# Kernel optimization log

Measured on AMD Instinct MI355X. Metric: run time of the kernel, lower is better.

Reference implementation:

```python
import jax, jax.numpy as jnp
import numpy as np

B, T, DF, S = 64, 16, 512, 196      # batch, ticks, backbone channels, tokens
D_IN, H = 512, 8                     # attention embed dim, heads
DH = D_IN // H
DM, MEM, HN = 1024, 25, 32           # d_model neurons, memory length, NLM hidden
NSA, NSO, DOUT = 512, 512, 512       # sync sizes (random-pairing), output dim


def _ln(x, g, b, eps=1e-5):
    m = x.mean(-1, keepdims=True)
    v = ((x - m) ** 2).mean(-1, keepdims=True)
    return (x - m) / jnp.sqrt(v + eps) * g + b


def setup_inputs() -> dict:
    key = jax.random.key(0)
    ks = jax.random.split(key, 24)
    rn = lambda k, sh, sc: jax.random.normal(k, sh, jnp.float32) * sc
    p = {}
    p['x'] = rn(ks[0], (B, T, DF, S), 1.0)
    # q_proj (LazyLinear: n_sync_action -> d_input)
    p['Wqp'] = rn(ks[1], (NSA, D_IN), (1.0 / NSA) ** 0.5); p['bqp'] = jnp.zeros((D_IN,))
    # kv_proj: LazyLinear(DF->D_IN) + LayerNorm
    p['Wkv'] = rn(ks[2], (DF, D_IN), (1.0 / DF) ** 0.5); p['bkv'] = jnp.zeros((D_IN,))
    p['g_kv'] = jnp.ones((D_IN,)); p['b_kv'] = jnp.zeros((D_IN,))
    # MultiheadAttention projections
    sc = (1.0 / D_IN) ** 0.5
    p['Wq'] = rn(ks[3], (D_IN, D_IN), sc); p['bq'] = jnp.zeros((D_IN,))
    p['Wk'] = rn(ks[4], (D_IN, D_IN), sc); p['bk'] = jnp.zeros((D_IN,))
    p['Wv'] = rn(ks[5], (D_IN, D_IN), sc); p['bv'] = jnp.zeros((D_IN,))
    p['Wo'] = rn(ks[6], (D_IN, D_IN), sc); p['bo'] = jnp.zeros((D_IN,))
    # synapses: Linear(D_IN+DM -> 2*DM) + GLU + LayerNorm(DM)
    p['Wsyn'] = rn(ks[7], (D_IN + DM, 2 * DM), (1.0 / (D_IN + DM)) ** 0.5)
    p['bsyn'] = jnp.zeros((2 * DM,))
    p['g_syn'] = jnp.ones((DM,)); p['b_syn'] = jnp.zeros((DM,))
    # NLM: per-neuron 2-layer MLP over memory window
    p['W1'] = rn(ks[8], (DM, MEM, HN), (1.0 / MEM) ** 0.5); p['b1'] = jnp.zeros((DM, HN))
    p['W2'] = rn(ks[9], (DM, HN), (1.0 / HN) ** 0.5); p['b2'] = jnp.zeros((DM,))
    # learned initial states
    p['init_act'] = rn(ks[10], (DM,), (1.0 / DM) ** 0.5)
    p['init_hist'] = rn(ks[11], (DM, MEM), (1.0 / (DM + MEM)) ** 0.5)
    # decay params (init zero in torch)
    p['decay_a'] = jnp.zeros((NSA,)); p['decay_o'] = jnp.zeros((NSO,))
    # output projection (LazyLinear: n_sync_out -> d_output)
    p['Wout'] = rn(ks[12], (NSO, DOUT), (1.0 / NSO) ** 0.5); p['bout'] = jnp.zeros((DOUT,))
    # random-pairing neuron indices (buffers, constants)
    p['li_a'] = jax.random.randint(ks[13], (NSA,), 0, DM, jnp.int32)
    p['ri_a'] = jax.random.randint(ks[14], (NSA,), 0, DM, jnp.int32)
    p['li_o'] = jax.random.randint(ks[15], (NSO,), 0, DM, jnp.int32)
    p['ri_o'] = jax.random.randint(ks[16], (NSO,), 0, DM, jnp.int32)
    return p


def reference(x, Wqp, bqp, Wkv, bkv, g_kv, b_kv, Wq, bq, Wk, bk, Wv, bv, Wo, bo,
              Wsyn, bsyn, g_syn, b_syn, W1, b1, W2, b2, init_act, init_hist,
              decay_a, decay_o, Wout, bout, li_a, ri_a, li_o, ri_o):
    r_a = jnp.exp(-jnp.clip(decay_a, 0.0, 15.0))   # [NSA]
    r_o = jnp.exp(-jnp.clip(decay_o, 0.0, 15.0))   # [NSO]
    act0 = jnp.broadcast_to(init_act, (B, DM))
    hist0 = jnp.broadcast_to(init_hist, (B, DM, MEM))
    # initial 'out' sync state (decay_alpha=pairwise, decay_beta=ones)
    ao0 = act0[:, li_o] * act0[:, ri_o]
    bo0 = jnp.ones_like(ao0)
    # 'action' state starts None -> zeros so first update gives alpha=pairwise, beta=1
    aa0 = jnp.zeros((B, NSA), x.dtype); ba0 = jnp.zeros((B, NSA), x.dtype)

    def mha(q, kv):
        # q [B,1,D_IN], kv [B,S,D_IN]
        qh = (q @ Wq + bq).reshape(B, 1, H, DH)
        kh = (kv @ Wk + bk).reshape(B, S, H, DH)
        vh = (kv @ Wv + bv).reshape(B, S, H, DH)
        sc = jnp.einsum('bqhd,bkhd->bhqk', qh, kh) / jnp.sqrt(jnp.float32(DH))
        a = jax.nn.softmax(sc, axis=-1)
        o = jnp.einsum('bhqk,bkhd->bqhd', a, vh).reshape(B, 1, D_IN)
        return o @ Wo + bo

    def tick(carry, xt):
        act, hist, aa, ba, ao, bo_ = carry
        # compute_kv: identity backbone, flatten(2).transpose(1,2) -> [B,S,DF]
        kv = _ln(jnp.swapaxes(xt, 1, 2) @ Wkv + bkv, g_kv, b_kv)
        # action sync
        aa = r_a * aa + act[:, li_a] * act[:, ri_a]
        ba = r_a * ba + 1.0
        sync_a = aa / jnp.sqrt(ba)
        q = (sync_a @ Wqp + bqp)[:, None, :]
        attn = mha(q, kv)[:, 0]                         # [B,D_IN]
        pre = jnp.concatenate([attn, act], axis=-1)     # [B,D_IN+DM]
        g = pre @ Wsyn + bsyn
        a_, b_ = jnp.split(g, 2, axis=-1)
        pre_act = _ln(a_ * jax.nn.sigmoid(b_), g_syn, b_syn)  # [B,DM]
        hist = jnp.concatenate([hist[:, :, 1:], pre_act[:, :, None]], axis=2)
        # NLM: per-neuron MLP over memory window
        h = jax.nn.relu(jnp.einsum('bnm,nmh->bnh', hist, W1) + b1)
        act = jnp.einsum('bnh,nh->bn', h, W2) + b2
        # out sync
        ao = r_o * ao + act[:, li_o] * act[:, ri_o]
        bo_ = r_o * bo_ + 1.0
        sync_o = ao / jnp.sqrt(bo_)
        pred = sync_o @ Wout + bout                      # [B,DOUT]
        logp = jax.nn.log_softmax(pred, axis=-1)
        ne = -(jnp.exp(logp) * logp).sum(-1) / jnp.log(jnp.float32(DOUT))
        cert = jnp.stack([ne, 1.0 - ne], axis=-1)        # [B,2]
        return (act, hist, aa, ba, ao, bo_), (pred, cert)

    xt = jnp.moveaxis(x, 1, 0)  # [T,B,DF,S]
    _, (preds, certs) = jax.lax.scan(tick, (act0, hist0, aa0, ba0, ao0, bo0), xt)
    predictions = jnp.moveaxis(preds, 0, -1)   # [B,DOUT,T]
    certainties = jnp.moveaxis(certs, 0, -1)   # [B,2,T]
    return predictions, certainties
```

## Files before the change

kernel.cpp:

```cpp
#include <hip/hip_runtime.h>
#include <stdint.h>
#include <stddef.h>

#define B_    64
#define T_    16
#define DF_   512
#define S_    196
#define DIN_  512
#define H_    8
#define DH_   64
#define DM_   1024
#define MEM_  25
#define HN_   32
#define MR_   (B_*S_)
#define TC_   4
#define MCC_  (MR_*TC_)

typedef short bf16x8 __attribute__((ext_vector_type(8)));
typedef short short4v __attribute__((ext_vector_type(4)));
typedef float f32x4  __attribute__((ext_vector_type(4)));

__device__ __forceinline__ float b2f(short h){
  unsigned u = ((unsigned)(unsigned short)h) << 16;
  float f; __builtin_memcpy(&f, &u, 4); return f;
}
__device__ __forceinline__ short f2b(float f){
  unsigned u; __builtin_memcpy(&u, &f, 4);
  u = (u + 0x7fffu + ((u >> 16) & 1u)) >> 16;
  return (short)(unsigned short)u;
}
__device__ __forceinline__ float clip015(float d){
  return d < 0.f ? 0.f : (d > 15.f ? 15.f : d);
}

template<int OUTF32, int LNEPI>
__device__ __forceinline__ void gemm_body(int tid, int bx, int by, int aload,
    short* lA, short* lB,
    const short* __restrict__ A, const short* __restrict__ WT,
    void* __restrict__ Cout,
    const float* __restrict__ biasA, const float* __restrict__ biasB, int nsplit,
    const float* __restrict__ mu, const float* __restrict__ iv,
    const float* __restrict__ gw, const float* __restrict__ bw,
    int M, int N, int K, int lda, int ldc)
{
  const int w = tid >> 6, l = tid & 63;
  const int m0 = bx * 128, n0 = by * 128;
  const int wm = (w >> 1) * 64, wn = (w & 1) * 64;
  f32x4 acc[4][4];
  #pragma unroll
  for (int i=0;i<4;i++)
    #pragma unroll
    for (int j=0;j<4;j++) acc[i][j] = (f32x4){0.f,0.f,0.f,0.f};

  for (int k0 = 0; k0 < K; k0 += 64) {
    #pragma unroll
    for (int rnd = 0; rnd < 4; ++rnd) {
      int cb = (rnd*4 + w) * 64;
      int slot = cb + l;
      int row = slot >> 3, kb = slot & 7;
      int kc = k0 + ((kb ^ (row & 7)) << 3);
      if (aload) {
        int gm = m0 + row; if (gm > M-1) gm = M-1;
        __builtin_amdgcn_global_load_lds(
            (const __attribute__((address_space(1))) void*)(A + (size_t)gm * lda + kc),
            (__attribute__((address_space(3))) void*)&lA[cb*8], 16, 0, 0);
      }
      __builtin_amdgcn_global_load_lds(
          (const __attribute__((address_space(1))) void*)(WT + (size_t)(n0 + row) * K + kc),
          (__attribute__((address_space(3))) void*)&lB[cb*8], 16, 0, 0);
    }
    asm volatile("s_waitcnt vmcnt(0)" ::: "memory");
    __syncthreads();
    #pragma unroll
    for (int ks = 0; ks < 2; ++ks) {
      bf16x8 af[4], bfr[4];
      #pragma unroll
      for (int i = 0; i < 4; ++i) {
        int ra = wm + i*16 + (l & 15);
        int c  = ks*4 + (l >> 4);
        af[i]  = *(const bf16x8*)&lA[ra*64 + ((c ^ (ra & 7)) << 3)];
        int rb = wn + i*16 + (l & 15);
        bfr[i] = *(const bf16x8*)&lB[rb*64 + ((c ^ (rb & 7)) << 3)];
      }
      #pragma unroll
      for (int i = 0; i < 4; ++i)
        #pragma unroll
        for (int j = 0; j < 4; ++j)
          acc[i][j] = __builtin_amdgcn_mfma_f32_16x16x32_bf16(af[i], bfr[j], acc[i][j], 0, 0, 0);
    }
    __syncthreads();
  }
  #pragma unroll
  for (int i = 0; i < 4; ++i) {
    #pragma unroll
    for (int j = 0; j < 4; ++j) {
      int gn = n0 + wn + j*16 + (l & 15);
      float ivn = 0.f, mun = 0.f, bb = 0.f;
      if (LNEPI == 2) { ivn = iv[gn]; mun = mu[gn]; }
      else bb = biasA ? ((gn < nsplit) ? biasA[gn] : biasB[gn - nsplit]) : 0.f;
      #pragma unroll
      for (int r = 0; r < 4; ++r) {
        int gm = m0 + wm + i*16 + (l >> 4)*4 + r;
        if (gm < M) {
          float v;
          if (LNEPI == 2) v = ivn*(acc[i][j][r] - mun*gw[gm]) + bw[gm];
          else            v = acc[i][j][r] + bb;
          if (OUTF32) ((float*)Cout)[(size_t)gm * ldc + gn] = v;
          else        ((short*)Cout)[(size_t)gm * ldc + gn] = f2b(v);
        }
      }
    }
  }
}

template<int OUTF32, int LNEPI>
__global__ __launch_bounds__(256,2) void gemm_k(
    const short* __restrict__ A, const short* __restrict__ WT,
    void* __restrict__ Cout,
    const float* __restrict__ biasA, const float* __restrict__ biasB, int nsplit,
    const float* __restrict__ mu, const float* __restrict__ iv,
    const float* __restrict__ gw, const float* __restrict__ bw,
    int M, int N, int K, int lda, int ldc)
{
  __shared__ short lA[128*64];
  __shared__ short lB[128*64];
  gemm_body<OUTF32,LNEPI>(threadIdx.x, blockIdx.x, blockIdx.y, 1, lA, lB,
                          A, WT, Cout, biasA, biasB, nsplit, mu, iv, gw, bw,
                          M, N, K, lda, ldc);
}

__device__ __forceinline__ void run_piggy(int tid, int pb, int pop, int poff,
    char* pool,
    const short* __restrict__ xTn, const short* __restrict__ WkvT,
    const float* __restrict__ bkv,
    short* __restrict__ kvpN, float* __restrict__ muN, float* __restrict__ ivN,
    const short* __restrict__ WkkvT, const float* __restrict__ gw,
    const float* __restrict__ bw, short* __restrict__ KVTN, int McN)
{
  if (pop == 1) {
    int twin = tid >> 8;
    short* lA = (short*)pool;
    short* lB = (short*)(pool + 16384 + 16384*twin);
    int p = poff + pb; if (p > 783) p = 783;
    int bx = p % 392, byp = p / 392;
    gemm_body<0,0>(tid & 255, bx, byp*2 + twin, twin == 0, lA, lB,
                   xTn, WkvT, kvpN, bkv, bkv, 1 << 30,
                   nullptr, nullptr, nullptr, nullptr,
                   McN, 512, 512, 512, 512);
  } else if (pop == 2) {
    int blk = poff + pb;
    int w = tid >> 6, l = tid & 63;
    for (int i = 0; i < 8; ++i) {
      int r = blk*64 + i*8 + w;
      if (r < McN) {
        bf16x8 v8 = *(const bf16x8*)&kvpN[(size_t)r*512 + l*8];
        float s = 0.f, s2 = 0.f;
        #pragma unroll
        for (int j = 0; j < 8; ++j) { float v = b2f(v8[j]); s += v; s2 += v*v; }
        #pragma unroll
        for (int m = 1; m < 64; m <<= 1) { s += __shfl_xor(s, m, 64); s2 += __shfl_xor(s2, m, 64); }
        if (l == 0) {
          float mean = s * (1.f/512.f);
          float var  = s2 * (1.f/512.f) - mean*mean;
          muN[r] = mean;
          ivN[r] = rsqrtf(var + 1e-5f);
        }
      }
    }
  } else if (pop == 3) {
    int twin = tid >> 8;
    short* lA = (short*)pool;
    short* lB = (short*)(pool + 16384 + 16384*twin);
    int p = poff + pb; if (p > 1567) p = 1567;
    int bx = p % 8, byp = p / 8;
    gemm_body<0,2>(tid & 255, bx, byp*2 + twin, twin == 0, lA, lB,
                   WkkvT, kvpN, KVTN, nullptr, nullptr, 0,
                   muN, ivN, gw, bw, 1024, McN, 512, 512, McN);
  }
}

__device__ __forceinline__ void attn_body(int b, int tid, float* smem,
    const float* actT, float* aa, float* ba,
    const int* li_a, const int* ri_a, const float* decay_a,
    const short* WqqB, const float* bqh,
    const short* KVT, int ldkv, int ti, short* preb)
{
  float* syncL = smem;
  float* qhL   = smem + 512;
  float* pL    = smem + 1024;
  int j = tid;
  float rr = expf(-clip015(decay_a[j]));
  float prod = actT[li_a[j]*64 + b] * actT[ri_a[j]*64 + b];
  float a2 = rr*aa[b*512+j] + prod; aa[b*512+j] = a2;
  float bb2 = rr*ba[b*512+j] + 1.f;  ba[b*512+j] = bb2;
  syncL[j] = a2 * rsqrtf(bb2);
  __syncthreads();
  float qa = bqh[j];
  #pragma unroll 8
  for (int k = 0; k < 512; ++k) qa += syncL[k]*b2f(WqqB[k*512+j]);
  qhL[j] = qa;
  __syncthreads();
  int h = tid >> 6, l = tid & 63;
  const size_t cb = (size_t)(ti*B_ + b) * S_;
  const short* Kb = KVT + (size_t)(h*64)*ldkv + cb;
  int s3 = 192 + l; int s3c = s3 < S_ ? s3 : S_-1;
  float sc0=0.f, sc1=0.f, sc2=0.f, sc3=0.f;
  #pragma unroll 8
  for (int d = 0; d < 64; ++d) {
    const short* kr = Kb + (size_t)d*ldkv;
    float qv = qhL[h*64 + d];
    sc0 += qv * b2f(kr[l]);
    sc1 += qv * b2f(kr[64 + l]);
    sc2 += qv * b2f(kr[128 + l]);
    sc3 += qv * b2f(kr[s3c]);
  }
  sc0 *= 0.125f; sc1 *= 0.125f; sc2 *= 0.125f;
  sc3 = (s3 < S_) ? sc3*0.125f : -1e30f;
  float mx = fmaxf(fmaxf(sc0, sc1), fmaxf(sc2, sc3));
  #pragma unroll
  for (int k = 32; k >= 1; k >>= 1) mx = fmaxf(mx, __shfl_xor(mx, k, 64));
  float p0 = expf(sc0-mx), p1 = expf(sc1-mx), p2 = expf(sc2-mx), p3 = expf(sc3-mx);
  pL[h*256 + l] = p0; pL[h*256 + 64+l] = p1;
  pL[h*256 + 128+l] = p2; pL[h*256 + 192+l] = p3;
  float ps = p0+p1+p2+p3;
  #pragma unroll
  for (int k = 32; k >= 1; k >>= 1) ps += __shfl_xor(ps, k, 64);
  float inv = 1.f / ps;
  __syncthreads();
  const short4v* vrow = (const short4v*)(KVT + (size_t)(512 + h*64 + l)*ldkv + cb);
  const float* pp = pL + h*256;
  float ac0=0.f, ac1=0.f, ac2=0.f, ac3=0.f;
  #pragma unroll 7
  for (int c = 0; c < 49; ++c) {
    short4v v4 = vrow[c];
    ac0 += pp[c*4]   * b2f(v4.x);
    ac1 += pp[c*4+1] * b2f(v4.y);
    ac2 += pp[c*4+2] * b2f(v4.z);
    ac3 += pp[c*4+3] * b2f(v4.w);
  }
  float accv = (ac0+ac1)+(ac2+ac3);
  preb[(size_t)b*1536 + h*64 + l] = f2b(accv * inv);
}

__device__ __forceinline__ void outk_body(int tt, int b, int tid,
    float* syncL, float* wred,
    const float* actT, float* ao, float* bo_s,
    const int* li_o, const int* ri_o, const float* decay_o,
    const short* WoutB, const float* bout, float* out)
{
  int j = tid;
  float rr = expf(-clip015(decay_o[j]));
  float prod = actT[li_o[j]*64 + b] * actT[ri_o[j]*64 + b];
  float a2 = rr*ao[b*512+j] + prod; ao[b*512+j] = a2;
  float bb2 = rr*bo_s[b*512+j] + 1.f; bo_s[b*512+j] = bb2;
  syncL[j] = a2 * rsqrtf(bb2);
  __syncthreads();
  float a = bout[j];
  #pragma unroll 8
  for (int k = 0; k < 512; ++k) a += syncL[k]*b2f(WoutB[k*512+j]);
  out[((size_t)b*512 + j)*16 + tt] = a;
  int w = tid >> 6, l = tid & 63;
  float m = a;
  #pragma unroll
  for (int k = 32; k >= 1; k >>= 1) m = fmaxf(m, __shfl_xor(m, k, 64));
  if (l == 0) wred[w] = m;
  __syncthreads();
  float M = wred[0];
  #pragma unroll
  for (int k = 1; k < 8; ++k) M = fmaxf(M, wred[k]);
  float e = expf(a - M);
  float z = e, s1 = e*(a - M);
  #pragma unroll
  for (int k = 32; k >= 1; k >>= 1) { z += __shfl_xor(z, k, 64); s1 += __shfl_xor(s1, k, 64); }
  if (l == 0) { wred[8+w] = z; wred[16+w] = s1; }
  __syncthreads();
  if (tid == 0) {
    float Z = 0.f, S1 = 0.f;
    #pragma unroll
    for (int k = 0; k < 8; ++k) { Z += wred[8+k]; S1 += wred[16+k]; }
    float plp = S1 / Z - logf(Z);
    float ne = -plp * (1.f/logf(512.f));
    out[524288 + (size_t)b*32 + tt]      = ne;
    out[524288 + (size_t)b*32 + 16 + tt] = 1.f - ne;
  }
}

__device__ __forceinline__ void synglu_body(int bid, int tid, char* pool,
    const short* preb, const short* WsynP, const float* bsynF, float* u)
{
  f32x4* part = (f32x4*)pool;
  int w = tid >> 6, l = tid & 63;
  int mf = w & 3, kh = w >> 2;
  int arow = mf*16 + (l & 15);
  int kbase = kh*768 + (l >> 4)*8;
  const short* ap = preb + (size_t)arow*1536 + kbase;
  const short* bp = WsynP + (size_t)(bid*16 + (l & 15))*1536 + kbase;
  f32x4 acc = (f32x4){0.f,0.f,0.f,0.f};
  #pragma unroll 4
  for (int ks = 0; ks < 24; ++ks) {
    bf16x8 av = *(const bf16x8*)(ap + ks*32);
    bf16x8 bv = *(const bf16x8*)(bp + ks*32);
    acc = __builtin_amdgcn_mfma_f32_16x16x32_bf16(av, bv, acc, 0, 0, 0);
  }
  part[w*64 + l] = acc;
  __syncthreads();
  if (w < 4) {
    f32x4 o1 = part[w*64 + l], o2 = part[(w+4)*64 + l];
    int c = l & 15;
    int colg = bid*8 + (c & 7);
    float bias = (c < 8) ? bsynF[colg] : bsynF[1024 + colg];
    float tv[4], pv[4];
    #pragma unroll
    for (int r2 = 0; r2 < 4; ++r2) tv[r2] = o1[r2] + o2[r2] + bias;
    #pragma unroll
    for (int r2 = 0; r2 < 4; ++r2) pv[r2] = __shfl_xor(tv[r2], 8, 64);
    if (c < 8) {
      #pragma unroll
      for (int r2 = 0; r2 < 4; ++r2) {
        float uu = tv[r2] * (1.f/(1.f + expf(-pv[r2])));
        int brow = w*16 + (l >> 4)*4 + r2;
        u[brow*1024 + colg] = uu;
      }
    }
  }
}

__device__ __forceinline__ void nlmln_body(int bid, int tid, char* pool,
    const float* u, const float* gsyn, const float* bln, float* hist,
    const float* W1, const float* b1, const float* W2, const float* b2,
    float* actT, short* preb, int t)
{
  float* mstat = (float*)pool;
  float* istat = mstat + 64;
  {
    int b = tid >> 3, p = tid & 7;
    const float* up = u + b*1024 + p*128;
    float s = 0.f, s2 = 0.f;
    #pragma unroll 8
    for (int i = 0; i < 128; ++i) { float v = up[i]; s += v; s2 += v*v; }
    #pragma unroll
    for (int k = 4; k >= 1; k >>= 1) { s += __shfl_xor(s, k, 64); s2 += __shfl_xor(s2, k, 64); }
    if (p == 0) {
      float mean = s * (1.f/1024.f);
      float var  = s2 * (1.f/1024.f) - mean*mean;
      mstat[b] = mean;
      istat[b] = rsqrtf(var + 1e-5f);
    }
  }
  __syncthreads();
  int n = (bid << 3) + (tid >> 6), b = tid & 63;
  float nv = (u[b*1024 + n] - mstat[b]) * istat[b] * gsyn[n] + bln[n];
  int slot = t % MEM_;
  hist[((size_t)n*MEM_ + slot)*64 + b] = nv;
  float h[32];
  #pragma unroll
  for (int j = 0; j < 32; ++j) h[j] = b1[n*32+j];
  #pragma unroll 5
  for (int m = 0; m < MEM_; ++m) {
    int phys = (t + 1 + m) % MEM_;
    float hv = (m == MEM_-1) ? nv : hist[((size_t)n*MEM_ + phys)*64 + b];
    const float* wp = &W1[((size_t)n*MEM_ + m)*32];
    #pragma unroll
    for (int j = 0; j < 32; ++j) h[j] += hv * wp[j];
  }
  float acc = b2[n];
  #pragma unroll
  for (int j = 0; j < 32; ++j) acc += fmaxf(h[j], 0.f) * W2[n*32+j];
  actT[n*64 + b] = acc;
  preb[(size_t)b*1536 + 512 + n] = f2b(acc);
}

#define PIGGY_ARGS int pop, int poff, \
    const short* __restrict__ xTn, const short* __restrict__ WkvT, \
    const float* __restrict__ bkv, short* __restrict__ kvpN, \
    float* __restrict__ muN, float* __restrict__ ivN, \
    const short* __restrict__ WkkvT, const float* __restrict__ gw, \
    const float* __restrict__ bw, short* __restrict__ KVTN, int McN
#define PIGGY_CALL run_piggy(tid, (int)blockIdx.x - 128, pop, poff, pool, \
    xTn, WkvT, bkv, kvpN, muN, ivN, WkkvT, gw, bw, KVTN, McN)

__global__ __launch_bounds__(512) void stageA(
    const float* __restrict__ actT,
    float* __restrict__ aa, float* __restrict__ ba,
    const int* __restrict__ li_a, const int* __restrict__ ri_a,
    const float* __restrict__ decay_a,
    const short* __restrict__ WqqB, const float* __restrict__ bqh,
    const short* __restrict__ KVT, int ldkv, int ti,
    short* __restrict__ preb,
    float* __restrict__ ao, float* __restrict__ bo_s,
    const int* __restrict__ li_o, const int* __restrict__ ri_o,
    const float* __restrict__ decay_o,
    const short* __restrict__ WoutB, const float* __restrict__ bout,
    float* __restrict__ out, int t, PIGGY_ARGS)
{
  __shared__ __attribute__((aligned(16))) char pool[49152];
  const int bid = blockIdx.x, tid = threadIdx.x;
  if (bid < 128) {
    float* smem = (float*)pool;
    if (bid < 64)
      attn_body(bid, tid, smem, actT, aa, ba, li_a, ri_a, decay_a,
                WqqB, bqh, KVT, ldkv, ti, preb);
    else if (t > 0)
      outk_body(t-1, bid-64, tid, smem, smem+512, actT, ao, bo_s,
                li_o, ri_o, decay_o, WoutB, bout, out);
  } else {
    PIGGY_CALL;
  }
}

__global__ __launch_bounds__(512) void stageB(
    const short* __restrict__ preb, const short* __restrict__ WsynP,
    const float* __restrict__ bsynF, float* __restrict__ u, PIGGY_ARGS)
{
  __shared__ __attribute__((aligned(16))) char pool[49152];
  const int bid = blockIdx.x, tid = threadIdx.x;
  if (bid < 128) synglu_body(bid, tid, pool, preb, WsynP, bsynF, u);
  else PIGGY_CALL;
}

__global__ __launch_bounds__(512) void stageC(
    const float* __restrict__ u, const float* __restrict__ gsyn,
    const float* __restrict__ bln, float* __restrict__ hist,
    const float* __restrict__ W1, const float* __restrict__ b1,
    const float* __restrict__ W2, const float* __restrict__ b2,
    float* __restrict__ actT, short* __restrict__ preb, int t, PIGGY_ARGS)
{
  __shared__ __attribute__((aligned(16))) char pool[49152];
  const int bid = blockIdx.x, tid = threadIdx.x;
  if (bid < 128) nlmln_body(bid, tid, pool, u, gsyn, bln, hist,
                            W1, b1, W2, b2, actT, preb, t);
  else PIGGY_CALL;
}

__global__ __launch_bounds__(512) void outk_fin(
    const float* __restrict__ actT,
    float* __restrict__ ao, float* __restrict__ bo_s,
    const int* __restrict__ li_o, const int* __restrict__ ri_o,
    const float* __restrict__ decay_o,
    const short* __restrict__ WoutB, const float* __restrict__ bout,
    float* __restrict__ out)
{
  __shared__ __attribute__((aligned(16))) float smem[544];
  outk_body(T_-1, blockIdx.x, threadIdx.x, smem, smem+512, actT, ao, bo_s,
            li_o, ri_o, decay_o, WoutB, bout, out);
}

__global__ __launch_bounds__(256) void xpose_x(const float* __restrict__ x,
                                               short* __restrict__ xT)
{
  __shared__ float tile[32][33];
  int df0 = blockIdx.x*32, s0 = blockIdx.y*32;
  int z = blockIdx.z;
  int b = z / T_, t = z % T_;
  int tx = threadIdx.x & 31, ty = threadIdx.x >> 5;
  const float* src = x + (size_t)(b*T_ + t) * DF_ * S_;
  #pragma unroll
  for (int i = 0; i < 4; ++i) {
    int df = df0 + ty + i*8;
    int s  = s0 + tx;
    tile[ty+i*8][tx] = (s < S_) ? src[(size_t)df*S_ + s] : 0.f;
  }
  __syncthreads();
  short* dst = xT + (size_t)(t*B_ + b) * S_ * DIN_;
  #pragma unroll
  for (int i = 0; i < 4; ++i) {
    int s  = s0 + ty + i*8;
    int df = df0 + tx;
    if (s < S_) dst[(size_t)s*DF_ + df] = f2b(tile[tx][ty+i*8]);
  }
}

__global__ __launch_bounds__(256) void wtrans(const float* __restrict__ in,
    short* __restrict__ out, int R, int C, int ldo, int coff,
    const float* __restrict__ scale)
{
  __shared__ float tile[32][33];
  int c0 = blockIdx.x*32, r0 = blockIdx.y*32;
  int tx = threadIdx.x & 31, ty = threadIdx.x >> 5;
  #pragma unroll
  for (int i = 0; i < 4; ++i) {
    int r = r0+ty+i*8;
    float sc = scale ? scale[r] : 1.f;
    tile[ty+i*8][tx] = in[(size_t)r*C + c0+tx] * sc;
  }
  __syncthreads();
  #pragma unroll
  for (int i = 0; i < 4; ++i)
    out[(size_t)(c0+ty+i*8)*ldo + coff + r0+tx] = f2b(tile[tx][ty+i*8]);
}

__global__ __launch_bounds__(256) void cvtb(const float* __restrict__ in,
                                            short* __restrict__ out, int n)
{
  int i = blockIdx.x*256 + threadIdx.x;
  if (i < n) out[i] = f2b(in[i]);
}

__global__ __launch_bounds__(256) void bias_fold(const float* __restrict__ vec,
    const float* __restrict__ W, const float* __restrict__ base,
    float* __restrict__ out, int N, int ldw)
{
  int n = blockIdx.x*256 + threadIdx.x;
  if (n >= N) return;
  float a = base ? base[n] : 0.f;
  #pragma unroll 8
  for (int k = 0; k < 512; ++k) a += vec[k]*W[(size_t)k*ldw + n];
  out[n] = a;
}

__global__ __launch_bounds__(256) void permrows(const short* __restrict__ in,
                                                short* __restrict__ out)
{
  int r = blockIdx.x;
  int k = r >> 4, i = r & 15;
  int src = (i < 8) ? (k*8 + i) : (1024 + k*8 + (i - 8));
  const bf16x8* s = (const bf16x8*)(in + (size_t)src*1536);
  bf16x8* d = (bf16x8*)(out + (size_t)r*1536);
  int j = threadIdx.x;
  if (j < 192) d[j] = s[j];
}

__global__ __launch_bounds__(256) void ln_stats(const short* __restrict__ in,
    float* __restrict__ mu, float* __restrict__ iv, int nrows)
{
  int w = threadIdx.x >> 6, l = threadIdx.x & 63;
  int r = blockIdx.x*4 + w;
  if (r >= nrows) return;
  bf16x8 v8 = *(const bf16x8*)&in[(size_t)r*512 + l*8];
  float s = 0.f, s2 = 0.f;
  #pragma unroll
  for (int j = 0; j < 8; ++j) { float v = b2f(v8[j]); s += v; s2 += v*v; }
  #pragma unroll
  for (int m = 1; m < 64; m <<= 1) { s += __shfl_xor(s, m, 64); s2 += __shfl_xor(s2, m, 64); }
  if (l == 0) {
    float mean = s * (1.f/512.f);
    float var  = s2 * (1.f/512.f) - mean*mean;
    mu[r] = mean;
    iv[r] = rsqrtf(var + 1e-5f);
  }
}

__global__ __launch_bounds__(256) void initk(float* __restrict__ aa, float* __restrict__ ba,
    float* __restrict__ ao, float* __restrict__ bo_s,
    float* __restrict__ actT, float* __restrict__ hist, short* __restrict__ preb,
    const float* __restrict__ init_act, const float* __restrict__ init_hist,
    const int* __restrict__ li_o, const int* __restrict__ ri_o)
{
  int i = blockIdx.x*256 + threadIdx.x;
  if (i < 64*512) {
    aa[i] = 0.f; ba[i] = 0.f;
    int j = i & 511;
    ao[i] = init_act[li_o[j]] * init_act[ri_o[j]];
    bo_s[i] = 1.f;
  }
  if (i < 65536) {
    int n = i >> 6, b = i & 63;
    actT[i] = init_act[n];
    preb[(size_t)b*1536 + 512 + n] = f2b(init_act[n]);
  }
  if (i < DM_*MEM_*64) {
    int nm = i >> 6;
    hist[i] = init_hist[nm];
  }
}

extern "C" void kernel_launch(void* const* d_in, const int* in_sizes, int n_in,
                              void* d_out, int out_size, void* d_ws, size_t ws_size,
                              hipStream_t stream)
{
  (void)in_sizes; (void)n_in; (void)out_size;
  const float* x       = (const float*)d_in[0];
  const float* Wqp     = (const float*)d_in[1];
  const float* bqp     = (const float*)d_in[2];
  const float* Wkv     = (const float*)d_in[3];
  const float* bkv     = (const float*)d_in[4];
  const float* g_kv    = (const float*)d_in[5];
  const float* b_kv    = (const float*)d_in[6];
  const float* Wq      = (const float*)d_in[7];
  const float* bq      = (const float*)d_in[8];
  const float* Wk      = (const float*)d_in[9];
  const float* bk      = (const float*)d_in[10];
  const float* Wv      = (const float*)d_in[11];
  const float* bv      = (const float*)d_in[12];
  const float* Wo      = (const float*)d_in[13];
  const float* bo_p    = (const float*)d_in[14];
  const float* Wsyn    = (const float*)d_in[15];
  const float* bsyn    = (const float*)d_in[16];
  const float* g_syn   = (const float*)d_in[17];
  const float* b_syn   = (const float*)d_in[18];
  const float* W1      = (const float*)d_in[19];
  const float* b1      = (const float*)d_in[20];
  const float* W2      = (const float*)d_in[21];
  const float* b2      = (const float*)d_in[22];
  const float* init_act  = (const float*)d_in[23];
  const float* init_hist = (const float*)d_in[24];
  const float* decay_a = (const float*)d_in[25];
  const float* decay_o = (const float*)d_in[26];
  const float* Wout    = (const float*)d_in[27];
  const float* bout    = (const float*)d_in[28];
  const int* li_a = (const int*)d_in[29];
  const int* ri_a = (const int*)d_in[30];
  const int* li_o = (const int*)d_in[31];
  const int* ri_o = (const int*)d_in[32];

  char* ws = (char*)d_ws;
  size_t off = 0;
  auto alloc = [&](size_t bytes) { char* p = ws + off; off += (bytes + 255) & ~(size_t)255; return p; };
  short* WkvT   = (short*)alloc(512*512*2);
  short* WkkvT  = (short*)alloc(1024*512*2);
  short* WsynF  = (short*)alloc(2048*1536*2);
  short* WsynP  = (short*)alloc(2048*1536*2);
  short* WsynTt = (short*)alloc(2048*512*2);
  short* WqpB   = (short*)alloc(512*512*2);
  short* WqT    = (short*)alloc(512*512*2);
  short* WoB    = (short*)alloc(512*512*2);
  short* WqqB   = (short*)alloc(512*512*2);
  short* WoutB  = (short*)alloc(512*512*2);
  float* bqh    = (float*)alloc(512*4);
  float* bsynF  = (float*)alloc(2048*4);
  float* gw     = (float*)alloc(1024*4);
  float* bw     = (float*)alloc(1024*4);
  short* preb   = (short*)alloc(64*1536*2);
  float* u      = (float*)alloc(64*1024*4);
  float* aa     = (float*)alloc(64*512*4);
  float* ba     = (float*)alloc(64*512*4);
  float* ao     = (float*)alloc(64*512*4);
  float* bo_s   = (float*)alloc(64*512*4);
  float* actT   = (float*)alloc(1024*64*4);
  float* hist   = (float*)alloc((size_t)1024*25*64*4);
  size_t fixed_end = off;

  const size_t szXT  = (size_t)T_*MR_*512*2;
  const size_t szKVP = (size_t)MCC_*512*2;
  const size_t szKVT = (size_t)MCC_*1024*2;
  const size_t szST  = (size_t)MCC_*4;
  size_t need_full = fixed_end + szXT + 2*szKVP + 2*szKVT + 4*szST + 4096;
  bool pig_en = (ws_size >= need_full);

  short* xT = (short*)alloc(szXT);
  short* kvpB[2]; short* KVTB[2]; float* muB[2]; float* ivB[2];
  kvpB[0] = (short*)alloc(szKVP);
  KVTB[0] = (short*)alloc(szKVT);
  muB[0]  = (float*)alloc(szST);
  ivB[0]  = (float*)alloc(szST);
  if (pig_en) {
    kvpB[1] = (short*)alloc(szKVP);
    KVTB[1] = (short*)alloc(szKVT);
    muB[1]  = (float*)alloc(szST);
    ivB[1]  = (float*)alloc(szST);
  } else {
    kvpB[1] = kvpB[0]; KVTB[1] = KVTB[0]; muB[1] = muB[0]; ivB[1] = ivB[0];
  }

  const int BIG = 1 << 30;
  const float* FN = nullptr;

  initk<<<6400, 256, 0, stream>>>(aa, ba, ao, bo_s, actT, hist, preb,
                                  init_act, init_hist, li_o, ri_o);
  wtrans<<<dim3(16,16), 256, 0, stream>>>(Wkv, WkvT, 512, 512, 512, 0, nullptr);
  wtrans<<<dim3(16,16), 256, 0, stream>>>(Wk,  WkkvT, 512, 512, 512, 0, g_kv);
  wtrans<<<dim3(16,16), 256, 0, stream>>>(Wv,  WkkvT + (size_t)512*512, 512, 512, 512, 0, g_kv);
  wtrans<<<dim3(64,32), 256, 0, stream>>>(Wsyn + (size_t)512*2048, WsynF, 1024, 2048, 1536, 512, nullptr);
  wtrans<<<dim3(64,16), 256, 0, stream>>>(Wsyn, WsynTt, 512, 2048, 512, 0, nullptr);
  wtrans<<<dim3(16,16), 256, 0, stream>>>(Wq,  WqT, 512, 512, 512, 0, nullptr);
  cvtb<<<1024, 256, 0, stream>>>(Wqp, WqpB, 512*512);
  cvtb<<<1024, 256, 0, stream>>>(Wo,  WoB,  512*512);
  cvtb<<<1024, 256, 0, stream>>>(Wout, WoutB, 512*512);
  gemm_k<0,0><<<dim3(4,4), 256, 0, stream>>>(WqpB, WqT, WqqB, nullptr, nullptr, BIG,
                                             FN, FN, FN, FN, 512, 512, 512, 512, 512);
  gemm_k<0,0><<<dim3(16,4), 256, 0, stream>>>(WsynTt, WoB, WsynF, nullptr, nullptr, BIG,
                                              FN, FN, FN, FN, 2048, 512, 512, 512, 1536);
  permrows<<<2048, 256, 0, stream>>>(WsynF, WsynP);
  bias_fold<<<2, 256, 0, stream>>>(bqp,  Wq,   bq,   bqh,   512,  512);
  bias_fold<<<8, 256, 0, stream>>>(bo_p, Wsyn, bsyn, bsynF, 2048, 2048);
  bias_fold<<<2, 256, 0, stream>>>(g_kv, Wk, nullptr, gw,       512, 512);
  bias_fold<<<2, 256, 0, stream>>>(g_kv, Wv, nullptr, gw + 512, 512, 512);
  bias_fold<<<2, 256, 0, stream>>>(b_kv, Wk, bk, bw,       512, 512);
  bias_fold<<<2, 256, 0, stream>>>(b_kv, Wv, bv, bw + 512, 512, 512);

  xpose_x<<<dim3(16,7,B_*T_), 256, 0, stream>>>(x, xT);

  auto run_pipe = [&](int c, short* kvpP, float* muP, float* ivP, short* KVTP){
    const short* xTc = xT + (size_t)c*TC_*MR_*512;
    gemm_k<0,0><<<dim3(392,4), 256, 0, stream>>>(xTc, WkvT, kvpP, bkv, bkv, BIG,
                                                 FN, FN, FN, FN, MCC_, 512, 512, 512, 512);
    ln_stats<<<MCC_/4, 256, 0, stream>>>(kvpP, muP, ivP, MCC_);
    gemm_k<0,2><<<dim3(8,392), 256, 0, stream>>>(WkkvT, kvpP, KVTP, nullptr, nullptr, BIG,
                                                 muP, ivP, gw, bw, 1024, MCC_, 512, 512, MCC_);
  };

  auto pigcfg = [](int q, bool pig, int& op, int& pf, int& n){
    op = 0; pf = 0; n = 0;
    if (!pig) return;
    if (q < 4)      { op = 1; pf = q*196;     n = 196; }
    else if (q == 4){ op = 2; pf = 0;         n = 784; }
    else            { op = 3; pf = (q-5)*224; n = 224; }
  };

  run_pipe(0, kvpB[0], muB[0], ivB[0], KVTB[0]);

  for (int c = 0; c < 4; ++c) {
    int par = pig_en ? (c & 1) : 0;
    int nxt = pig_en ? (par ^ 1) : 0;
    if (!pig_en && c > 0) run_pipe(c, kvpB[0], muB[0], ivB[0], KVTB[0]);
    bool pig = pig_en && (c < 3);
    const short* xTn = (c < 3) ? xT + (size_t)(c+1)*TC_*MR_*512 : xT;
    for (int ti = 0; ti < TC_; ++ti) {
      int t = c*TC_ + ti;
      int op, pf, n;
      pigcfg(ti*3+0, pig, op, pf, n);
      stageA<<<128+n, 512, 0, stream>>>(actT, aa, ba, li_a, ri_a, decay_a,
          WqqB, bqh, KVTB[par], MCC_, ti, preb,
          ao, bo_s, li_o, ri_o, decay_o, WoutB, bout, (float*)d_out, t,
          op, pf, xTn, WkvT, bkv, kvpB[nxt], muB[nxt], ivB[nxt],
          WkkvT, gw, bw, KVTB[nxt], MCC_);
      pigcfg(ti*3+1, pig, op, pf, n);
      stageB<<<128+n, 512, 0, stream>>>(preb, WsynP, bsynF, u,
          op, pf, xTn, WkvT, bkv, kvpB[nxt], muB[nxt], ivB[nxt],
          WkkvT, gw, bw, KVTB[nxt], MCC_);
      pigcfg(ti*3+2, pig, op, pf, n);
      stageC<<<128+n, 512, 0, stream>>>(u, g_syn, b_syn, hist,
          W1, b1, W2, b2, actT, preb, t,
          op, pf, xTn, WkvT, bkv, kvpB[nxt], muB[nxt], ivB[nxt],
          WkkvT, gw, bw, KVTB[nxt], MCC_);
    }
  }
  outk_fin<<<64, 512, 0, stream>>>(actT, ao, bo_s, li_o, ri_o, decay_o,
                                   WoutB, bout, (float*)d_out);
}
```

Before: 2.443 ms.

## Move input transpose for future chunks into piggyback blocks of recurrent stages

The upfront transpose of x to bf16 now covers only the first chunk of 4 ticks. Each later chunk's transpose runs as a new piggyback operation inside the stageA/B/C launches of the previous chunk, ahead of the KV projection GEMM. The piggyback schedule is rebalanced to 12 slots: 2 transpose, 4 GEMM, 1 LN stats, 5 for the second GEMM. The aim is to hide the memory-bound transpose behind the latency-bound recurrent kernels, at the cost of more piggyback blocks competing with the critical-path blocks.

```diff
diff --git a/kernel.cpp b/kernel.cpp
--- a/kernel.cpp
+++ b/kernel.cpp
@@ -131,18 +131,48 @@
 
 __device__ __forceinline__ void run_piggy(int tid, int pb, int pop, int poff,
     char* pool,
-    const short* __restrict__ xTn, const short* __restrict__ WkvT,
-    const float* __restrict__ bkv,
+    const float* __restrict__ xg, int t0n, short* __restrict__ xT,
+    const short* __restrict__ WkvT, const float* __restrict__ bkv,
     short* __restrict__ kvpN, float* __restrict__ muN, float* __restrict__ ivN,
     const short* __restrict__ WkkvT, const float* __restrict__ gw,
     const float* __restrict__ bw, short* __restrict__ KVTN, int McN)
 {
-  if (pop == 1) {
+  if (pop == 4) {
+    int twin = tid >> 8, tid2 = tid & 255;
+    float* tile = (float*)(pool + twin*8448);
+    int tx = tid2 & 31, ty = tid2 >> 5;
+    int base = (poff + pb)*32 + twin*16;
+    for (int it = 0; it < 16; ++it) {
+      int gt = base + it;
+      int df0 = (gt & 15) * 32;
+      int r = gt >> 4;
+      int s0 = (r % 7) * 32;
+      int z = r / 7;
+      int b = z >> 2, ti = z & 3;
+      const float* src = xg + (size_t)(b*T_ + t0n + ti) * DF_ * S_;
+      #pragma unroll
+      for (int i = 0; i < 4; ++i) {
+        int df = df0 + ty + i*8;
+        int s  = s0 + tx;
+        tile[(ty+i*8)*33 + tx] = (s < S_) ? src[(size_t)df*S_ + s] : 0.f;
+      }
+      __syncthreads();
+      short* dst = xT + (size_t)((t0n + ti)*B_ + b) * S_ * DIN_;
+      #pragma unroll
+      for (int i = 0; i < 4; ++i) {
+        int s  = s0 + ty + i*8;
+        int df = df0 + tx;
+        if (s < S_) dst[(size_t)s*DF_ + df] = f2b(tile[tx*33 + ty+i*8]);
+      }
+      __syncthreads();
+    }
+  } else if (pop == 1) {
     int twin = tid >> 8;
     short* lA = (short*)pool;
     short* lB = (short*)(pool + 16384 + 16384*twin);
     int p = poff + pb; if (p > 783) p = 783;
     int bx = p % 392, byp = p / 392;
+    const short* xTn = xT + (size_t)t0n * MR_ * 512;
     gemm_body<0,0>(tid & 255, bx, byp*2 + twin, twin == 0, lA, lB,
                    xTn, WkvT, kvpN, bkv, bkv, 1 << 30,
                    nullptr, nullptr, nullptr, nullptr,
@@ -371,13 +401,14 @@
 }
 
 #define PIGGY_ARGS int pop, int poff, \
-    const short* __restrict__ xTn, const short* __restrict__ WkvT, \
+    const float* __restrict__ xg, int t0n, short* __restrict__ xTg, \
+    const short* __restrict__ WkvT, \
     const float* __restrict__ bkv, short* __restrict__ kvpN, \
     float* __restrict__ muN, float* __restrict__ ivN, \
     const short* __restrict__ WkkvT, const float* __restrict__ gw, \
     const float* __restrict__ bw, short* __restrict__ KVTN, int McN
 #define PIGGY_CALL run_piggy(tid, (int)blockIdx.x - 128, pop, poff, pool, \
-    xTn, WkvT, bkv, kvpN, muN, ivN, WkkvT, gw, bw, KVTN, McN)
+    xg, t0n, xTg, WkvT, bkv, kvpN, muN, ivN, WkkvT, gw, bw, KVTN, McN)
 
 __global__ __launch_bounds__(512) void stageA(
     const float* __restrict__ actT,
@@ -446,14 +477,14 @@
 }
 
 __global__ __launch_bounds__(256) void xpose_x(const float* __restrict__ x,
-                                               short* __restrict__ xT)
+                                               short* __restrict__ xT, int t0, int tc)
 {
   __shared__ float tile[32][33];
   int df0 = blockIdx.x*32, s0 = blockIdx.y*32;
   int z = blockIdx.z;
-  int b = z / T_, t = z % T_;
+  int b = z / tc, ti = z % tc;
   int tx = threadIdx.x & 31, ty = threadIdx.x >> 5;
-  const float* src = x + (size_t)(b*T_ + t) * DF_ * S_;
+  const float* src = x + (size_t)(b*T_ + t0 + ti) * DF_ * S_;
   #pragma unroll
   for (int i = 0; i < 4; ++i) {
     int df = df0 + ty + i*8;
@@ -461,7 +492,7 @@
     tile[ty+i*8][tx] = (s < S_) ? src[(size_t)df*S_ + s] : 0.f;
   }
   __syncthreads();
-  short* dst = xT + (size_t)(t*B_ + b) * S_ * DIN_;
+  short* dst = xT + (size_t)((t0 + ti)*B_ + b) * S_ * DIN_;
   #pragma unroll
   for (int i = 0; i < 4; ++i) {
     int s  = s0 + ty + i*8;
@@ -678,7 +709,10 @@
   bias_fold<<<2, 256, 0, stream>>>(b_kv, Wk, bk, bw,       512, 512);
   bias_fold<<<2, 256, 0, stream>>>(b_kv, Wv, bv, bw + 512, 512, 512);
 
-  xpose_x<<<dim3(16,7,B_*T_), 256, 0, stream>>>(x, xT);
+  if (pig_en)
+    xpose_x<<<dim3(16,7,B_*TC_), 256, 0, stream>>>(x, xT, 0, TC_);
+  else
+    xpose_x<<<dim3(16,7,B_*T_), 256, 0, stream>>>(x, xT, 0, T_);
 
   auto run_pipe = [&](int c, short* kvpP, float* muP, float* ivP, short* KVTP){
     const short* xTc = xT + (size_t)c*TC_*MR_*512;
@@ -692,9 +726,10 @@
   auto pigcfg = [](int q, bool pig, int& op, int& pf, int& n){
     op = 0; pf = 0; n = 0;
     if (!pig) return;
-    if (q < 4)      { op = 1; pf = q*196;     n = 196; }
-    else if (q == 4){ op = 2; pf = 0;         n = 784; }
-    else            { op = 3; pf = (q-5)*224; n = 224; }
+    if (q < 2)      { op = 4; pf = q*448;     n = 448; }
+    else if (q < 6) { op = 1; pf = (q-2)*196; n = 196; }
+    else if (q == 6){ op = 2; pf = 0;         n = 784; }
+    else            { op = 3; pf = (q-7)*314; n = 314; }
   };
 
   run_pipe(0, kvpB[0], muB[0], ivB[0], KVTB[0]);
@@ -704,7 +739,7 @@
     int nxt = pig_en ? (par ^ 1) : 0;
     if (!pig_en && c > 0) run_pipe(c, kvpB[0], muB[0], ivB[0], KVTB[0]);
     bool pig = pig_en && (c < 3);
-    const short* xTn = (c < 3) ? xT + (size_t)(c+1)*TC_*MR_*512 : xT;
+    int t0n = (c < 3) ? (c+1)*TC_ : 0;
     for (int ti = 0; ti < TC_; ++ti) {
       int t = c*TC_ + ti;
       int op, pf, n;
@@ -712,16 +747,16 @@
       stageA<<<128+n, 512, 0, stream>>>(actT, aa, ba, li_a, ri_a, decay_a,
           WqqB, bqh, KVTB[par], MCC_, ti, preb,
           ao, bo_s, li_o, ri_o, decay_o, WoutB, bout, (float*)d_out, t,
-          op, pf, xTn, WkvT, bkv, kvpB[nxt], muB[nxt], ivB[nxt],
+          op, pf, x, t0n, xT, WkvT, bkv, kvpB[nxt], muB[nxt], ivB[nxt],
           WkkvT, gw, bw, KVTB[nxt], MCC_);
       pigcfg(ti*3+1, pig, op, pf, n);
       stageB<<<128+n, 512, 0, stream>>>(preb, WsynP, bsynF, u,
-          op, pf, xTn, WkvT, bkv, kvpB[nxt], muB[nxt], ivB[nxt],
+          op, pf, x, t0n, xT, WkvT, bkv, kvpB[nxt], muB[nxt], ivB[nxt],
           WkkvT, gw, bw, KVTB[nxt], MCC_);
       pigcfg(ti*3+2, pig, op, pf, n);
       stageC<<<128+n, 512, 0, stream>>>(u, g_syn, b_syn, hist,
           W1, b1, W2, b2, actT, preb, t,
-          op, pf, xTn, WkvT, bkv, kvpB[nxt], muB[nxt], ivB[nxt],
+          op, pf, x, t0n, xT, WkvT, bkv, kvpB[nxt], muB[nxt], ivB[nxt],
           WkkvT, gw, bw, KVTB[nxt], MCC_);
     }
   }
```

New measurement: 2.346 ms. -4.0%, faster.
